# Performance work log

Measured on AMD Instinct MI355X. Metric: run time of the kernel, lower is better.

Reference implementation:

```python
import jax, jax.numpy as jnp
import numpy as np

N_NODES = 50000
N_EDGES = 1600000
IN_FEATS = 256
HIDDEN = 128
N_CLASSES = 40


def setup_inputs() -> dict:
    key = jax.random.key(0)
    k1, k2, k3, k4, k5, k6 = jax.random.split(key, 6)
    inputs = jax.random.normal(k1, (N_NODES, IN_FEATS), dtype=jnp.float32)
    src = jax.random.randint(k2, (N_EDGES,), 0, N_NODES, dtype=jnp.int64 if jax.config.jax_enable_x64 else jnp.int32)
    dst = jax.random.randint(k3, (N_EDGES,), 0, N_NODES, dtype=jnp.int64 if jax.config.jax_enable_x64 else jnp.int32)
    # glorot-style init for GraphConv weights, zero bias (DGL defaults)
    W1 = jax.random.normal(k4, (IN_FEATS, HIDDEN), dtype=jnp.float32) * (1.0 / np.sqrt(IN_FEATS))
    b1 = jnp.zeros((HIDDEN,), dtype=jnp.float32)
    W2 = jax.random.normal(k5, (HIDDEN, N_CLASSES), dtype=jnp.float32) * (1.0 / np.sqrt(HIDDEN))
    b2 = jnp.zeros((N_CLASSES,), dtype=jnp.float32)
    return {"inputs": inputs, "src": src, "dst": dst, "W1": W1, "b1": b1, "W2": W2, "b2": b2}


def _graph_conv(x, W, b, src, dst, deg_out_isqrt, deg_in_isqrt):
    # DGL GraphConv, norm='both': D_dst^{-1/2} A (D_src^{-1/2} X W) + b
    # W applied before aggregation (in_feats >= out_feats path)
    h = (x * deg_out_isqrt[:, None]) @ W                      # [N, out]
    msg = h[src]                                              # [E, out] gather
    agg = jax.ops.segment_sum(msg, dst, num_segments=x.shape[0])  # [N, out] scatter-add
    return agg * deg_in_isqrt[:, None] + b


def reference(inputs, src, dst, W1, b1, W2, b2):
    n = inputs.shape[0]
    ones = jnp.ones((src.shape[0],), dtype=inputs.dtype)
    deg_out = jax.ops.segment_sum(ones, src, num_segments=n)
    deg_in = jax.ops.segment_sum(ones, dst, num_segments=n)
    deg_out_isqrt = jnp.where(deg_out > 0, jax.lax.rsqrt(jnp.maximum(deg_out, 1.0)), 0.0)
    deg_in_isqrt = jnp.where(deg_in > 0, jax.lax.rsqrt(jnp.maximum(deg_in, 1.0)), 0.0)
    h = _graph_conv(inputs, W1, b1, src, dst, deg_out_isqrt, deg_in_isqrt)
    h = _graph_conv(h, W2, b2, src, dst, deg_out_isqrt, deg_in_isqrt)
    return jax.nn.log_softmax(h, axis=1)
```

## Files before the change

### kernel.cpp

```cpp
#include <hip/hip_runtime.h>
#include <math.h>

#define N_NODES 50000
#define N_EDGES 1600000
#define IN_F 256
#define HID 128
#define NCLS 40
#define HS2 40
#define NP 50048
#define NBINS 196
#define MS_BLOCKS 200
#define MS_CHUNK 8000
#define BIN_CAP 12288

typedef __attribute__((ext_vector_type(8))) short short8;
typedef __attribute__((ext_vector_type(4))) float v4f;
typedef __attribute__((ext_vector_type(2))) _Float16 h2v;

__device__ __forceinline__ unsigned short f2bf(float f) {
    union { float f; unsigned int i; } v;
    v.f = f;
    unsigned int r = v.i + 0x7FFF + ((v.i >> 16) & 1);
    return (unsigned short)(r >> 16);
}
__device__ __forceinline__ h2v u2h(unsigned int u) {
    union { unsigned int i; h2v h; } v; v.i = u; return v.h;
}
__device__ __forceinline__ unsigned int h2u(h2v h) {
    union { h2v h; unsigned int i; } v; v.h = h; return v.i;
}


__global__ __launch_bounds__(256) void k_init(int* __restrict__ cur_d,
                                              int* __restrict__ cur_s) {
    int t = threadIdx.x;
    if (t < NBINS) {
        cur_d[t] = t * BIN_CAP;
        cur_s[t] = t * BIN_CAP;
    }
}


__global__ __launch_bounds__(256) void k_ms(const int* __restrict__ src,
                                            const int* __restrict__ dst,
                                            int* __restrict__ cur_d, int* __restrict__ cur_s,
                                            int* __restrict__ binned_d,
                                            unsigned char* __restrict__ binned_s,
                                            const float* __restrict__ W1,
                                            const float* __restrict__ b1,
                                            const float* __restrict__ W2,
                                            short* __restrict__ w12f,
                                            float* __restrict__ b1w2) {
    __shared__ int smem[11024];
    int t = threadIdx.x;
    if (blockIdx.x < 2 * MS_BLOCKS) {
        int* hist  = smem;
        int* delta = smem + 256;
        int* lcur  = smem + 512;
        int* sm    = smem + 768;
        int* stage = smem + 1024;
        unsigned char* binof = (unsigned char*)(smem + 9024);
        int side = blockIdx.x / MS_BLOCKS;
        int e0 = (blockIdx.x % MS_BLOCKS) * MS_CHUNK;
        const int* key = side ? src : dst;
        for (int i = t; i < NBINS; i += 256) hist[i] = 0;
        __syncthreads();
        for (int i = t; i < MS_CHUNK; i += 256) atomicAdd(&hist[key[e0 + i] >> 8], 1);
        __syncthreads();
        int hv = (t < NBINS) ? hist[t] : 0;
        sm[t] = hv;
        __syncthreads();
        for (int off = 1; off < 256; off <<= 1) {
            int a = (t >= off) ? sm[t - off] : 0;
            __syncthreads();
            sm[t] += a;
            __syncthreads();
        }
        if (t < NBINS) {
            int ex = sm[t] - hv;
            int g = atomicAdd(side ? &cur_s[t] : &cur_d[t], hv);
            delta[t] = g - ex;
            lcur[t] = ex;
        }
        __syncthreads();
        if (side == 0) {
            for (int i = t; i < MS_CHUNK; i += 256) {
                int kf = key[e0 + i];
                int v = src[e0 + i];
                int b = kf >> 8;
                int pos = atomicAdd(&lcur[b], 1);
                stage[pos] = ((kf & 255) << 16) | v;
                binof[pos] = (unsigned char)b;
            }
            __syncthreads();
            for (int i = t; i < MS_CHUNK; i += 256)
                binned_d[i + delta[binof[i]]] = stage[i];
        } else {
            for (int i = t; i < MS_CHUNK; i += 256) {
                int kf = key[e0 + i];
                int b = kf >> 8;
                int pos = atomicAdd(&lcur[b], 1);
                stage[pos] = kf & 255;
                binof[pos] = (unsigned char)b;
            }
            __syncthreads();
            for (int i = t; i < MS_CHUNK; i += 256)
                binned_s[i + delta[binof[i]]] = (unsigned char)stage[i];
        }
        return;
    }
    if (blockIdx.x == 2 * MS_BLOCKS + 6) {
        int c = t;
        if (c < NCLS) {
            float a0 = 0.f, a1 = 0.f, a2 = 0.f, a3 = 0.f;
            for (int k = 0; k < HID; k += 4) {
                a0 += b1[k + 0] * W2[(k + 0) * NCLS + c];
                a1 += b1[k + 1] * W2[(k + 1) * NCLS + c];
                a2 += b1[k + 2] * W2[(k + 2) * NCLS + c];
                a3 += b1[k + 3] * W2[(k + 3) * NCLS + c];
            }
            b1w2[c] = (a0 + a1) + (a2 + a3);
        }
        return;
    }
    float* w2s = (float*)smem;
    for (int i = t; i < HID * NCLS; i += 256) w2s[i] = W2[i];
    __syncthreads();
    int g = (blockIdx.x - 2 * MS_BLOCKS) * 256 + t;
    int kt = g / 192, rem = g % 192;
    int nt = rem >> 6, lane = rem & 63;
    int q = lane >> 4, n = lane & 15;
    int col = nt * 16 + n;
    float acc[8];
#pragma unroll
    for (int j = 0; j < 8; j++) acc[j] = 0.f;
    if (col < NCLS) {
        int k0 = kt * 32 + q * 8;
        const float* w1r = &W1[(size_t)k0 * HID];
        for (int jj = 0; jj < HID; jj += 4) {
            float w0 = w2s[(jj + 0) * NCLS + col];
            float w1v = w2s[(jj + 1) * NCLS + col];
            float w2v = w2s[(jj + 2) * NCLS + col];
            float w3 = w2s[(jj + 3) * NCLS + col];
#pragma unroll
            for (int j = 0; j < 8; j++) {
                float4 a = *(const float4*)&w1r[j * HID + jj];
                acc[j] += a.x * w0 + a.y * w1v + a.z * w2v + a.w * w3;
            }
        }
    }
    short8 v;
#pragma unroll
    for (int j = 0; j < 8; j++) v[j] = (short)f2bf(acc[j]);
    *(short8*)&w12f[(size_t)g * 8] = v;
}


__global__ __launch_bounds__(256) void k_bins(const int* __restrict__ binned_d,
                                              const unsigned char* __restrict__ binned_s,
                                              const int* __restrict__ cur_d,
                                              const int* __restrict__ cur_s,
                                              int* __restrict__ offsets, float* __restrict__ din,
                                              float* __restrict__ dout,
                                              unsigned short* __restrict__ deg16,
                                              unsigned short* __restrict__ csr16) {
    __shared__ int hist[256];
    __shared__ int sm[256];
    __shared__ int cur[256];
    __shared__ int stage[BIN_CAP];
    int t = threadIdx.x;
    hist[t] = 0;
    __syncthreads();
    if (blockIdx.x < NBINS) {
        int bin = blockIdx.x;
        int beg = bin * BIN_CAP;
        int n = cur_d[bin] - beg;
        for (int i = t; i < n; i += 256) atomicAdd(&hist[binned_d[beg + i] >> 16], 1);
        __syncthreads();
        int hv = hist[t];
        sm[t] = hv;
        __syncthreads();
        for (int off = 1; off < 256; off <<= 1) {
            int a = (t >= off) ? sm[t - off] : 0;
            __syncthreads();
            sm[t] += a;
            __syncthreads();
        }
        int ex = sm[t] - hv;
        int node = bin * 256 + t;
        if (node < N_NODES) {
            offsets[node] = beg + ex;
            deg16[node] = (unsigned short)hv;
            din[node] = hv ? rsqrtf((float)hv) : 0.f;
        }
        cur[t] = ex;
        __syncthreads();
        for (int i = t; i < n; i += 256) {
            int p = binned_d[beg + i];
            int pos = atomicAdd(&cur[p >> 16], 1);
            if (pos < BIN_CAP) stage[pos] = p & 0xFFFF;
        }
        __syncthreads();
        int m = n < BIN_CAP ? n : BIN_CAP;
        for (int i = t; i < m; i += 256) csr16[beg + i] = (unsigned short)stage[i];
    } else {
        int bin = blockIdx.x - NBINS;
        int beg = bin * BIN_CAP;
        int n = cur_s[bin] - beg;
        for (int i = t; i < n; i += 256) atomicAdd(&hist[binned_s[beg + i]], 1);
        __syncthreads();
        int node = bin * 256 + t;
        if (node < N_NODES) {
            int hv2 = hist[t];
            dout[node] = hv2 ? rsqrtf((float)hv2) : 0.f;
        }
    }
}


__global__ __launch_bounds__(256) void k_gemm1(const float* __restrict__ x,
                                               const short* __restrict__ w12f,
                                               const float* __restrict__ dout,
                                               _Float16* __restrict__ gt) {
    int t = threadIdx.x;
    int wv = t >> 6, lane = t & 63;
    int q = lane >> 4, lr = lane & 15;
    int m0 = blockIdx.x * 64 + wv * 16;
    int row = m0 + lr;
    int rowc = min(row, N_NODES - 1);
    v4f acc[3];
#pragma unroll
    for (int n = 0; n < 3; n++) acc[n] = (v4f){0.f, 0.f, 0.f, 0.f};

    const float* xr = &x[(size_t)rowc * IN_F];
#pragma unroll
    for (int kt = 0; kt < 8; kt++) {
        const float4* ap = (const float4*)&xr[kt * 32 + q * 8];
        float4 a0 = ap[0], a1 = ap[1];
        short8 af;
        af[0] = (short)f2bf(a0.x); af[1] = (short)f2bf(a0.y);
        af[2] = (short)f2bf(a0.z); af[3] = (short)f2bf(a0.w);
        af[4] = (short)f2bf(a1.x); af[5] = (short)f2bf(a1.y);
        af[6] = (short)f2bf(a1.z); af[7] = (short)f2bf(a1.w);
#pragma unroll
        for (int nt = 0; nt < 3; nt++) {
            short8 bf = *(const short8*)&w12f[(size_t)((kt * 3 + nt) * 64 + lane) * 8];
            acc[nt] = __builtin_amdgcn_mfma_f32_16x16x32_bf16(af, bf, acc[nt], 0, 0, 0);
        }
    }
    int rbase = m0 + q * 4;
    float4 dv = *(const float4*)&dout[rbase];
#pragma unroll
    for (int i = 0; i < 4; i++) {
        int orow = rbase + i;
        if (orow < N_NODES) {
            float s = (i == 0) ? dv.x : (i == 1) ? dv.y : (i == 2) ? dv.z : dv.w;
#pragma unroll
            for (int nt = 0; nt < 3; nt++) {
                int col = nt * 16 + lr;
                if (col < NCLS)
                    gt[(size_t)orow * HS2 + col] = (_Float16)(acc[nt][i] * s);
            }
        }
    }
}


__global__ __launch_bounds__(256) void k_agg1b(const unsigned short* __restrict__ csr16,
                                               const int* __restrict__ offsets,
                                               const unsigned short* __restrict__ deg16,
                                               const _Float16* __restrict__ g,
                                               const float* __restrict__ din,
                                               const float* __restrict__ dout,
                                               const float* __restrict__ b1w2,
                                               _Float16* __restrict__ h2b) {
    int w = (int)((blockIdx.x * 256 + threadIdx.x) >> 6);
    int wid0 = w * 2;
    if (wid0 >= N_NODES) return;
    int wid1 = wid0 + 1;
    int lane = threadIdx.x & 63;
    int half = lane >> 5;
    int hl = lane & 31;
    int grp = hl >> 3;
    int l = hl & 7;
    bool act = l < 5;
    int colb = min(l, 4) * 8;
    int sbase = half << 5;
    int beg0 = offsets[wid0];
    int beg1 = offsets[wid1];
    unsigned int dp = *(const unsigned int*)&deg16[wid0];
    int end0 = beg0 + (int)(dp & 0xFFFFu);
    int end1 = beg1 + (int)(dp >> 16);
    int myend = half ? end1 : end0;
    h2v a0 = (h2v)0, a1 = (h2v)0, a2 = (h2v)0, a3 = (h2v)0;
    for (int base0 = beg0, base1 = beg1; base0 < end0 || base1 < end1;
         base0 += 32, base1 += 32) {
        int mybase = half ? base1 : base0;
        int idx = mybase + hl;
        int sv = (idx < myend) ? (int)csr16[idx] : 0;
        int mycnt = min(32, myend - mybase);
        int mycl = max(mycnt - 1, 0);
        int e0 = grp * 8 + 0, e1 = grp * 8 + 1, e2 = grp * 8 + 2, e3 = grp * 8 + 3;
        int e4 = grp * 8 + 4, e5 = grp * 8 + 5, e6 = grp * 8 + 6, e7 = grp * 8 + 7;
        int s0 = __shfl(sv, sbase + min(e0, mycl));
        int s1 = __shfl(sv, sbase + min(e1, mycl));
        int s2 = __shfl(sv, sbase + min(e2, mycl));
        int s3 = __shfl(sv, sbase + min(e3, mycl));
        int s4 = __shfl(sv, sbase + min(e4, mycl));
        int s5 = __shfl(sv, sbase + min(e5, mycl));
        int s6 = __shfl(sv, sbase + min(e6, mycl));
        int s7 = __shfl(sv, sbase + min(e7, mycl));
        if (act && mycnt > 0) {
            uint4 v0 = *(const uint4*)&g[(size_t)s0 * HS2 + colb];
            uint4 v1 = *(const uint4*)&g[(size_t)s1 * HS2 + colb];
            uint4 v2 = *(const uint4*)&g[(size_t)s2 * HS2 + colb];
            uint4 v3 = *(const uint4*)&g[(size_t)s3 * HS2 + colb];
            uint4 v4 = *(const uint4*)&g[(size_t)s4 * HS2 + colb];
            uint4 v5 = *(const uint4*)&g[(size_t)s5 * HS2 + colb];
            uint4 v6 = *(const uint4*)&g[(size_t)s6 * HS2 + colb];
            uint4 v7 = *(const uint4*)&g[(size_t)s7 * HS2 + colb];
            if (e0 < mycnt) { a0 += u2h(v0.x); a1 += u2h(v0.y); a2 += u2h(v0.z); a3 += u2h(v0.w); }
            if (e1 < mycnt) { a0 += u2h(v1.x); a1 += u2h(v1.y); a2 += u2h(v1.z); a3 += u2h(v1.w); }
            if (e2 < mycnt) { a0 += u2h(v2.x); a1 += u2h(v2.y); a2 += u2h(v2.z); a3 += u2h(v2.w); }
            if (e3 < mycnt) { a0 += u2h(v3.x); a1 += u2h(v3.y); a2 += u2h(v3.z); a3 += u2h(v3.w); }
            if (e4 < mycnt) { a0 += u2h(v4.x); a1 += u2h(v4.y); a2 += u2h(v4.z); a3 += u2h(v4.w); }
            if (e5 < mycnt) { a0 += u2h(v5.x); a1 += u2h(v5.y); a2 += u2h(v5.z); a3 += u2h(v5.w); }
            if (e6 < mycnt) { a0 += u2h(v6.x); a1 += u2h(v6.y); a2 += u2h(v6.z); a3 += u2h(v6.w); }
            if (e7 < mycnt) { a0 += u2h(v7.x); a1 += u2h(v7.y); a2 += u2h(v7.z); a3 += u2h(v7.w); }
        }
    }
    float c[8];
    c[0] = (float)a0[0]; c[1] = (float)a0[1];
    c[2] = (float)a1[0]; c[3] = (float)a1[1];
    c[4] = (float)a2[0]; c[5] = (float)a2[1];
    c[6] = (float)a3[0]; c[7] = (float)a3[1];
#pragma unroll
    for (int i = 0; i < 8; i++) {
        c[i] += __shfl_xor(c[i], 8);
        c[i] += __shfl_xor(c[i], 16);
    }
    if (grp == 0 && act) {
        int wid = half ? wid1 : wid0;
        float dd = dout[wid];
        float sc = din[wid] * dd;
        float4 bw0 = *(const float4*)&b1w2[colb];
        float4 bw1 = *(const float4*)&b1w2[colb + 4];
        h2v p0, p1, p2, p3;
        p0[0] = (_Float16)(c[0] * sc + bw0.x * dd); p0[1] = (_Float16)(c[1] * sc + bw0.y * dd);
        p1[0] = (_Float16)(c[2] * sc + bw0.z * dd); p1[1] = (_Float16)(c[3] * sc + bw0.w * dd);
        p2[0] = (_Float16)(c[4] * sc + bw1.x * dd); p2[1] = (_Float16)(c[5] * sc + bw1.y * dd);
        p3[0] = (_Float16)(c[6] * sc + bw1.z * dd); p3[1] = (_Float16)(c[7] * sc + bw1.w * dd);
        uint4 o;
        o.x = h2u(p0); o.y = h2u(p1); o.z = h2u(p2); o.w = h2u(p3);
        *(uint4*)&h2b[(size_t)wid * HS2 + colb] = o;
    }
}


__global__ __launch_bounds__(256) void k_agg2(const unsigned short* __restrict__ csr16,
                                              const int* __restrict__ offsets,
                                              const unsigned short* __restrict__ deg16,
                                              const _Float16* __restrict__ h2b,
                                              const float* __restrict__ din,
                                              const float* __restrict__ b2,
                                              float* __restrict__ out) {
    int w = (int)((blockIdx.x * 256 + threadIdx.x) >> 6);
    int wid0 = w * 2;
    if (wid0 >= N_NODES) return;
    int wid1 = wid0 + 1;
    int lane = threadIdx.x & 63;
    int half = lane >> 5;
    int hl = lane & 31;
    int grp = hl >> 3;
    int l = hl & 7;
    bool act = l < 5;
    int colb = min(l, 4) * 8;
    int sbase = half << 5;
    int beg0 = offsets[wid0];
    int beg1 = offsets[wid1];
    unsigned int dp = *(const unsigned int*)&deg16[wid0];
    int end0 = beg0 + (int)(dp & 0xFFFFu);
    int end1 = beg1 + (int)(dp >> 16);
    int myend = half ? end1 : end0;
    h2v a0 = (h2v)0, a1 = (h2v)0, a2 = (h2v)0, a3 = (h2v)0;
    for (int base0 = beg0, base1 = beg1; base0 < end0 || base1 < end1;
         base0 += 32, base1 += 32) {
        int mybase = half ? base1 : base0;
        int idx = mybase + hl;
        int sv = (idx < myend) ? (int)csr16[idx] : 0;
        int mycnt = min(32, myend - mybase);
        int mycl = max(mycnt - 1, 0);
        int e0 = grp * 8 + 0, e1 = grp * 8 + 1, e2 = grp * 8 + 2, e3 = grp * 8 + 3;
        int e4 = grp * 8 + 4, e5 = grp * 8 + 5, e6 = grp * 8 + 6, e7 = grp * 8 + 7;
        int s0 = __shfl(sv, sbase + min(e0, mycl));
        int s1 = __shfl(sv, sbase + min(e1, mycl));
        int s2 = __shfl(sv, sbase + min(e2, mycl));
        int s3 = __shfl(sv, sbase + min(e3, mycl));
        int s4 = __shfl(sv, sbase + min(e4, mycl));
        int s5 = __shfl(sv, sbase + min(e5, mycl));
        int s6 = __shfl(sv, sbase + min(e6, mycl));
        int s7 = __shfl(sv, sbase + min(e7, mycl));
        if (act && mycnt > 0) {
            uint4 v0 = *(const uint4*)&h2b[(size_t)s0 * HS2 + colb];
            uint4 v1 = *(const uint4*)&h2b[(size_t)s1 * HS2 + colb];
            uint4 v2 = *(const uint4*)&h2b[(size_t)s2 * HS2 + colb];
            uint4 v3 = *(const uint4*)&h2b[(size_t)s3 * HS2 + colb];
            uint4 v4 = *(const uint4*)&h2b[(size_t)s4 * HS2 + colb];
            uint4 v5 = *(const uint4*)&h2b[(size_t)s5 * HS2 + colb];
            uint4 v6 = *(const uint4*)&h2b[(size_t)s6 * HS2 + colb];
            uint4 v7 = *(const uint4*)&h2b[(size_t)s7 * HS2 + colb];
            if (e0 < mycnt) { a0 += u2h(v0.x); a1 += u2h(v0.y); a2 += u2h(v0.z); a3 += u2h(v0.w); }
            if (e1 < mycnt) { a0 += u2h(v1.x); a1 += u2h(v1.y); a2 += u2h(v1.z); a3 += u2h(v1.w); }
            if (e2 < mycnt) { a0 += u2h(v2.x); a1 += u2h(v2.y); a2 += u2h(v2.z); a3 += u2h(v2.w); }
            if (e3 < mycnt) { a0 += u2h(v3.x); a1 += u2h(v3.y); a2 += u2h(v3.z); a3 += u2h(v3.w); }
            if (e4 < mycnt) { a0 += u2h(v4.x); a1 += u2h(v4.y); a2 += u2h(v4.z); a3 += u2h(v4.w); }
            if (e5 < mycnt) { a0 += u2h(v5.x); a1 += u2h(v5.y); a2 += u2h(v5.z); a3 += u2h(v5.w); }
            if (e6 < mycnt) { a0 += u2h(v6.x); a1 += u2h(v6.y); a2 += u2h(v6.z); a3 += u2h(v6.w); }
            if (e7 < mycnt) { a0 += u2h(v7.x); a1 += u2h(v7.y); a2 += u2h(v7.z); a3 += u2h(v7.w); }
        }
    }
    float c[8];
    c[0] = (float)a0[0]; c[1] = (float)a0[1];
    c[2] = (float)a1[0]; c[3] = (float)a1[1];
    c[4] = (float)a2[0]; c[5] = (float)a2[1];
    c[6] = (float)a3[0]; c[7] = (float)a3[1];
#pragma unroll
    for (int i = 0; i < 8; i++) {
        c[i] += __shfl_xor(c[i], 8);
        c[i] += __shfl_xor(c[i], 16);
    }
    int wid = half ? wid1 : wid0;
    float sc = din[wid];
    float y[8];
    float lm = -INFINITY;
    if (act) {
        float4 bb0 = *(const float4*)&b2[colb];
        float4 bb1 = *(const float4*)&b2[colb + 4];
        y[0] = c[0] * sc + bb0.x; y[1] = c[1] * sc + bb0.y;
        y[2] = c[2] * sc + bb0.z; y[3] = c[3] * sc + bb0.w;
        y[4] = c[4] * sc + bb1.x; y[5] = c[5] * sc + bb1.y;
        y[6] = c[6] * sc + bb1.z; y[7] = c[7] * sc + bb1.w;
#pragma unroll
        for (int i = 0; i < 8; i++) lm = fmaxf(lm, y[i]);
    }
#pragma unroll
    for (int off = 1; off < 8; off <<= 1) lm = fmaxf(lm, __shfl_xor(lm, off));
    float ls = 0.f;
    if (act) {
#pragma unroll
        for (int i = 0; i < 8; i++) ls += expf(y[i] - lm);
    }
#pragma unroll
    for (int off = 1; off < 8; off <<= 1) ls += __shfl_xor(ls, off);
    if (grp == 0 && act) {
        float lg = logf(ls);
        float4 o0 = make_float4(y[0] - lm - lg, y[1] - lm - lg, y[2] - lm - lg, y[3] - lm - lg);
        float4 o1 = make_float4(y[4] - lm - lg, y[5] - lm - lg, y[6] - lm - lg, y[7] - lm - lg);
        *(float4*)&out[(size_t)wid * NCLS + colb] = o0;
        *(float4*)&out[(size_t)wid * NCLS + colb + 4] = o1;
    }
}


extern "C" void kernel_launch(void* const* d_in, const int* in_sizes, int n_in,
                              void* d_out, int out_size, void* d_ws, size_t ws_size,
                              hipStream_t stream) {
    const float* x  = (const float*)d_in[0];
    const int* src  = (const int*)d_in[1];
    const int* dst  = (const int*)d_in[2];
    const float* W1 = (const float*)d_in[3];
    const float* b1 = (const float*)d_in[4];
    const float* W2 = (const float*)d_in[5];
    const float* b2 = (const float*)d_in[6];
    float* out = (float*)d_out;

    int* wsi   = (int*)d_ws;
    float* wsf = (float*)d_ws;
    const size_t BINREG = (size_t)NBINS * BIN_CAP;
    int* cur_d    = wsi;
    int* cur_s    = wsi + 256;
    float* b1w2   = wsf + 512;
    int* offsets  = wsi + 1536;
    float* din    = wsf + 1536 + (size_t)NP;
    float* dout   = wsf + 1536 + 2 * (size_t)NP;
    unsigned short* deg16 = (unsigned short*)(wsi + 1536 + 3 * (size_t)NP);
    int* binned_d = wsi + 1536 + 3 * (size_t)NP + NP / 2;
    unsigned char* binned_s = (unsigned char*)(binned_d + BINREG);
    _Float16* gt  = (_Float16*)(binned_s + BINREG);
    _Float16* h2b = gt + (size_t)N_NODES * HS2;
    short* w12f   = (short*)(h2b + (size_t)N_NODES * HS2);
    unsigned short* csr16 = (unsigned short*)(w12f + 12288);

    k_init<<<1, 256, 0, stream>>>(cur_d, cur_s);
    k_ms<<<2 * MS_BLOCKS + 7, 256, 0, stream>>>(src, dst, cur_d, cur_s, binned_d, binned_s,
                                                W1, b1, W2, w12f, b1w2);
    k_bins<<<2 * NBINS, 256, 0, stream>>>(binned_d, binned_s, cur_d, cur_s,
                                          offsets, din, dout, deg16, csr16);
    k_gemm1<<<(N_NODES + 63) / 64, 256, 0, stream>>>(x, w12f, dout, gt);
    k_agg1b<<<(N_NODES / 2) * 64 / 256, 256, 0, stream>>>(csr16, offsets, deg16, gt, din, dout, b1w2, h2b);
    k_agg2<<<(N_NODES / 2) * 64 / 256, 256, 0, stream>>>(csr16, offsets, deg16, h2b, din, b2, out);
}
```

Before: 193.1 us.

## Fuse CSR bin sort with GEMM1 launch and split out-degree kernel

New measurement: 198.6 us. 2.8% more time.

```diff
diff --git a/kernel.cpp b/kernel.cpp
--- a/kernel.cpp
+++ b/kernel.cpp
@@ -12,6 +12,7 @@
 #define MS_BLOCKS 200
 #define MS_CHUNK 8000
 #define BIN_CAP 12288
+#define GEMM_BLOCKS 782
 
 typedef __attribute__((ext_vector_type(8))) short short8;
 typedef __attribute__((ext_vector_type(4))) float v4f;
@@ -51,15 +52,16 @@
                                             const float* __restrict__ W2,
                                             short* __restrict__ w12f,
                                             float* __restrict__ b1w2) {
-    __shared__ int smem[11024];
+    __shared__ int smem[9024];
     int t = threadIdx.x;
     if (blockIdx.x < 2 * MS_BLOCKS) {
         int* hist  = smem;
         int* delta = smem + 256;
         int* lcur  = smem + 512;
         int* sm    = smem + 768;
-        int* stage = smem + 1024;
-        unsigned char* binof = (unsigned char*)(smem + 9024);
+        unsigned short* stage_s = (unsigned short*)(smem + 1024);
+        unsigned char*  stage_b = (unsigned char*)(smem + 5024);
+        unsigned char*  binof   = (unsigned char*)(smem + 7024);
         int side = blockIdx.x / MS_BLOCKS;
         int e0 = (blockIdx.x % MS_BLOCKS) * MS_CHUNK;
         const int* key = side ? src : dst;
@@ -89,23 +91,24 @@
                 int v = src[e0 + i];
                 int b = kf >> 8;
                 int pos = atomicAdd(&lcur[b], 1);
-                stage[pos] = ((kf & 255) << 16) | v;
+                stage_s[pos] = (unsigned short)v;
+                stage_b[pos] = (unsigned char)(kf & 255);
                 binof[pos] = (unsigned char)b;
             }
             __syncthreads();
             for (int i = t; i < MS_CHUNK; i += 256)
-                binned_d[i + delta[binof[i]]] = stage[i];
+                binned_d[i + delta[binof[i]]] = ((int)stage_b[i] << 16) | (int)stage_s[i];
         } else {
             for (int i = t; i < MS_CHUNK; i += 256) {
                 int kf = key[e0 + i];
                 int b = kf >> 8;
                 int pos = atomicAdd(&lcur[b], 1);
-                stage[pos] = kf & 255;
+                stage_b[pos] = (unsigned char)(kf & 255);
                 binof[pos] = (unsigned char)b;
             }
             __syncthreads();
             for (int i = t; i < MS_CHUNK; i += 256)
-                binned_s[i + delta[binof[i]]] = (unsigned char)stage[i];
+                binned_s[i + delta[binof[i]]] = stage_b[i];
         }
         return;
     }
@@ -156,22 +159,43 @@
 }
 
 
-__global__ __launch_bounds__(256) void k_bins(const int* __restrict__ binned_d,
-                                              const unsigned char* __restrict__ binned_s,
-                                              const int* __restrict__ cur_d,
+__global__ __launch_bounds__(256) void k_dout(const unsigned char* __restrict__ binned_s,
                                               const int* __restrict__ cur_s,
-                                              int* __restrict__ offsets, float* __restrict__ din,
-                                              float* __restrict__ dout,
-                                              unsigned short* __restrict__ deg16,
-                                              unsigned short* __restrict__ csr16) {
+                                              float* __restrict__ dout) {
+    __shared__ int hist[256];
+    int t = threadIdx.x;
+    hist[t] = 0;
+    __syncthreads();
+    int bin = blockIdx.x;
+    int beg = bin * BIN_CAP;
+    int n = cur_s[bin] - beg;
+    for (int i = t; i < n; i += 256) atomicAdd(&hist[binned_s[beg + i]], 1);
+    __syncthreads();
+    int node = bin * 256 + t;
+    if (node < N_NODES) {
+        int hv = hist[t];
+        dout[node] = hv ? rsqrtf((float)hv) : 0.f;
+    }
+}
+
+
+__global__ __launch_bounds__(256) void k_sg(const int* __restrict__ binned_d,
+                                            const int* __restrict__ cur_d,
+                                            int* __restrict__ offsets, float* __restrict__ din,
+                                            unsigned short* __restrict__ deg16,
+                                            unsigned short* __restrict__ csr16,
+                                            const float* __restrict__ x,
+                                            const short* __restrict__ w12f,
+                                            const float* __restrict__ dout,
+                                            _Float16* __restrict__ gt) {
     __shared__ int hist[256];
     __shared__ int sm[256];
     __shared__ int cur[256];
-    __shared__ int stage[BIN_CAP];
+    __shared__ unsigned short stage16[BIN_CAP];
     int t = threadIdx.x;
-    hist[t] = 0;
-    __syncthreads();
     if (blockIdx.x < NBINS) {
+        hist[t] = 0;
+        __syncthreads();
         int bin = blockIdx.x;
         int beg = bin * BIN_CAP;
         int n = cur_d[bin] - beg;
@@ -198,34 +222,19 @@
         for (int i = t; i < n; i += 256) {
             int p = binned_d[beg + i];
             int pos = atomicAdd(&cur[p >> 16], 1);
-            if (pos < BIN_CAP) stage[pos] = p & 0xFFFF;
+            if (pos < BIN_CAP) stage16[pos] = (unsigned short)(p & 0xFFFF);
         }
         __syncthreads();
         int m = n < BIN_CAP ? n : BIN_CAP;
-        for (int i = t; i < m; i += 256) csr16[beg + i] = (unsigned short)stage[i];
-    } else {
-        int bin = blockIdx.x - NBINS;
-        int beg = bin * BIN_CAP;
-        int n = cur_s[bin] - beg;
-        for (int i = t; i < n; i += 256) atomicAdd(&hist[binned_s[beg + i]], 1);
-        __syncthreads();
-        int node = bin * 256 + t;
-        if (node < N_NODES) {
-            int hv2 = hist[t];
-            dout[node] = hv2 ? rsqrtf((float)hv2) : 0.f;
-        }
-    }
-}
-
-
-__global__ __launch_bounds__(256) void k_gemm1(const float* __restrict__ x,
-                                               const short* __restrict__ w12f,
-                                               const float* __restrict__ dout,
-                                               _Float16* __restrict__ gt) {
-    int t = threadIdx.x;
+        int mw = (m + 1) >> 1;
+        unsigned int* dp = (unsigned int*)&csr16[beg];
+        const unsigned int* sp = (const unsigned int*)stage16;
+        for (int i = t; i < mw; i += 256) dp[i] = sp[i];
+        return;
+    }
     int wv = t >> 6, lane = t & 63;
     int q = lane >> 4, lr = lane & 15;
-    int m0 = blockIdx.x * 64 + wv * 16;
+    int m0 = (blockIdx.x - NBINS) * 64 + wv * 16;
     int row = m0 + lr;
     int rowc = min(row, N_NODES - 1);
     v4f acc[3];
@@ -494,9 +503,9 @@
     k_init<<<1, 256, 0, stream>>>(cur_d, cur_s);
     k_ms<<<2 * MS_BLOCKS + 7, 256, 0, stream>>>(src, dst, cur_d, cur_s, binned_d, binned_s,
                                                 W1, b1, W2, w12f, b1w2);
-    k_bins<<<2 * NBINS, 256, 0, stream>>>(binned_d, binned_s, cur_d, cur_s,
-                                          offsets, din, dout, deg16, csr16);
-    k_gemm1<<<(N_NODES + 63) / 64, 256, 0, stream>>>(x, w12f, dout, gt);
+    k_dout<<<NBINS, 256, 0, stream>>>(binned_s, cur_s, dout);
+    k_sg<<<NBINS + GEMM_BLOCKS, 256, 0, stream>>>(binned_d, cur_d, offsets, din, deg16, csr16,
+                                                  x, w12f, dout, gt);
     k_agg1b<<<(N_NODES / 2) * 64 / 256, 256, 0, stream>>>(csr16, offsets, deg16, gt, din, dout, b1w2, h2b);
     k_agg2<<<(N_NODES / 2) * 64 / 256, 256, 0, stream>>>(csr16, offsets, deg16, h2b, din, b2, out);
 }
```
